# Kernel optimization log

Measured on AMD Instinct MI355X. Metric: run time of the kernel, lower is better.

## Reference

```python
import jax, jax.numpy as jnp
import numpy as np

H = 512          # hidden_size
E = 2 * H        # bidirectional embed dim
NH = 8           # attention heads
HD = E // NH     # head dim = 128
SEQ = 10         # hard-coded seq_len in forward
IN = 512         # input_size
OUT = 256        # output_size


def _gru_dir(gi, Whh, bhh, reverse):
    # gi: [B,S,3H] precomputed input-side gate pre-activations
    if reverse:
        gi = gi[:, ::-1]
    B = gi.shape[0]
    h0 = jnp.zeros((B, H), gi.dtype)

    def step(h, gi_t):
        gh = h @ Whh.T + bhh                      # [B,3H]
        ir, iz, inn = jnp.split(gi_t, 3, axis=-1)
        hr, hz, hn = jnp.split(gh, 3, axis=-1)
        r = jax.nn.sigmoid(ir + hr)
        z = jax.nn.sigmoid(iz + hz)
        n = jnp.tanh(inn + r * hn)
        h_new = (1.0 - z) * n + z * h
        return h_new, h_new

    _, hs = jax.lax.scan(step, h0, jnp.swapaxes(gi, 0, 1))
    hs = jnp.swapaxes(hs, 0, 1)                   # [B,S,H]
    if reverse:
        hs = hs[:, ::-1]
    return hs


def _bi_gru_layer(x_seq, Wih, Whh, bih, bhh):
    # Wih: [2, 3H, in]; dir 0 = forward, dir 1 = backward
    outs = []
    for d, rev in ((0, False), (1, True)):
        gi = jnp.einsum('bsi,gi->bsg', x_seq, Wih[d]) + bih[d]
        outs.append(_gru_dir(gi, Whh[d], bhh[d], rev))
    return jnp.concatenate(outs, axis=-1)         # [B,S,2H]


def _attention(x, in_proj_w, in_proj_b, out_proj_w, out_proj_b):
    B, S, _ = x.shape
    qkv = x @ in_proj_w.T + in_proj_b             # [B,S,3E]
    q, k, v = jnp.split(qkv, 3, axis=-1)
    q = q.reshape(B, S, NH, HD)
    k = k.reshape(B, S, NH, HD)
    v = v.reshape(B, S, NH, HD)
    scores = jnp.einsum('bqhd,bkhd->bhqk', q, k) / jnp.sqrt(jnp.asarray(HD, x.dtype))
    attn = jax.nn.softmax(scores, axis=-1)
    o = jnp.einsum('bhqk,bkhd->bqhd', attn, v).reshape(B, S, E)
    return o @ out_proj_w.T + out_proj_b


def _forward(x, Wp, bp, Wih0, Whh0, bih0, bhh0, Wih1, Whh1, bih1, bhh1,
             in_proj_w, in_proj_b, out_proj_w, out_proj_b, W1, b1, W2, b2):
    x_proj = x @ Wp.T + bp                        # [B,H]
    phases = 2.0 * np.pi * np.arange(SEQ) / SEQ
    cos = jnp.asarray(np.cos(phases), x.dtype)    # [S]
    sin = jnp.asarray(np.sin(phases), x.dtype)
    rolled = jnp.roll(x_proj, shift=1, axis=-1)
    x_seq = (x_proj[:, None, :] * (1.0 + 0.1 * cos[None, :, None])
             + 0.05 * sin[None, :, None] * rolled[:, None, :])  # [B,S,H]
    h1 = _bi_gru_layer(x_seq, Wih0, Whh0, bih0, bhh0)           # [B,S,2H]
    gru_out = _bi_gru_layer(h1, Wih1, Whh1, bih1, bhh1)         # [B,S,2H]
    attn_out = _attention(gru_out, in_proj_w, in_proj_b, out_proj_w, out_proj_b)
    aggregated = jnp.mean(gru_out + attn_out, axis=1)           # [B,2H]
    hid = jnp.tanh(aggregated @ W1.T + b1)                      # [B,128]
    return hid @ W2.T + b2                                      # [B,OUT]


def setup_inputs() -> dict:
    key = jax.random.key(0)
    ks = jax.random.split(key, 24)
    s = 1.0 / np.sqrt(H)
    u = lambda k, shape: jax.random.uniform(k, shape, jnp.float32, -s, s)
    return {
        'x': jax.random.normal(ks[0], (4096, IN), jnp.float32),
        'Wp': u(ks[1], (H, IN)), 'bp': u(ks[2], (H,)),
        'Wih0': u(ks[3], (2, 3 * H, H)), 'Whh0': u(ks[4], (2, 3 * H, H)),
        'bih0': u(ks[5], (2, 3 * H)), 'bhh0': u(ks[6], (2, 3 * H)),
        'Wih1': u(ks[7], (2, 3 * H, 2 * H)), 'Whh1': u(ks[8], (2, 3 * H, H)),
        'bih1': u(ks[9], (2, 3 * H)), 'bhh1': u(ks[10], (2, 3 * H)),
        'in_proj_w': u(ks[11], (3 * E, E)), 'in_proj_b': u(ks[12], (3 * E,)),
        'out_proj_w': u(ks[13], (E, E)), 'out_proj_b': u(ks[14], (E,)),
        'W1': u(ks[15], (128, E)), 'b1': u(ks[16], (128,)),
        'W2': u(ks[17], (OUT, 128)), 'b2': u(ks[18], (OUT,)),
    }


def reference(x, Wp, bp, Wih0, Whh0, bih0, bhh0, Wih1, Whh1, bih1, bhh1,
              in_proj_w, in_proj_b, out_proj_w, out_proj_b, W1, b1, W2, b2):
    return _forward(x, Wp, bp, Wih0, Whh0, bih0, bhh0, Wih1, Whh1, bih1, bhh1,
                    in_proj_w, in_proj_b, out_proj_w, out_proj_b, W1, b1, W2, b2)
```

## Files before the change

### kernel.cpp

```cpp
#include <hip/hip_runtime.h>
#include <math.h>


#define SEQ 10

typedef unsigned short bf16u;
typedef __attribute__((ext_vector_type(8))) short short8v;
typedef __attribute__((ext_vector_type(4))) float f32x4;

__device__ __forceinline__ float b2f(bf16u u) {
    union { unsigned int i; float f; } v; v.i = ((unsigned int)u) << 16; return v.f;
}
__device__ __forceinline__ bf16u f2b(float f) {
    union { float f; unsigned int i; } v; v.f = f;
    unsigned int r = (v.i + 0x7FFFu + ((v.i >> 16) & 1u)) >> 16;
    return (bf16u)r;
}
__device__ __forceinline__ float fast_sigm(float x) { return 1.0f / (1.0f + __expf(-x)); }
__device__ __forceinline__ float fast_tanh(float x) {
    float e = __expf(-2.0f * x);
    return 2.0f / (1.0f + e) - 1.0f;
}

__global__ void cvt_f2b(const float* __restrict__ src, bf16u* __restrict__ dst, int n4)
{
    int i = blockIdx.x * 256 + threadIdx.x;
    if (i < n4) {
        float4 v = ((const float4*)src)[i];
        ushort4 u; u.x = f2b(v.x); u.y = f2b(v.y); u.z = f2b(v.z); u.w = f2b(v.w);
        ((ushort4*)dst)[i] = u;
    }
}

template <typename TC>
__global__ __launch_bounds__(256) void gemm_mfma(
    const bf16u* __restrict__ A, long long sAz, int lda,
    const bf16u* __restrict__ W, long long sWz,
    const float* __restrict__ bias, long long sBz,
    TC* __restrict__ C, long long sCz, int ldc,
    int K, int act)
{
    __shared__ bf16u As[128 * 64];
    __shared__ bf16u Ws[128 * 64];

    const int z = blockIdx.z;
    A += (long long)z * sAz;
    W += (long long)z * sWz;
    C += (long long)z * sCz;
    const float* bz = bias ? (bias + (long long)z * sBz) : nullptr;

    const int gx = gridDim.x;
    const int nwg = gx * gridDim.y;
    const int orig = blockIdx.y * gx + blockIdx.x;
    const int q = nwg >> 3, rres = nwg & 7;
    const int xcd = orig & 7, loc = orig >> 3;
    const int wgid = (xcd < rres ? xcd * (q + 1) : rres * (q + 1) + (xcd - rres) * q) + loc;
    const int bm = (wgid / gx) * 128;
    const int bn = (wgid % gx) * 128;

    const int tid = threadIdx.x;
    const int lane = tid & 63;
    const int wave = tid >> 6;
    const int wr = (wave >> 1) * 64;
    const int wc = (wave & 1) * 64;
    const int l15 = lane & 15;
    const int lk8 = (lane >> 4) * 8;

    f32x4 acc[4][4];
#pragma unroll
    for (int i = 0; i < 4; ++i)
#pragma unroll
        for (int j = 0; j < 4; ++j)
#pragma unroll
            for (int r = 0; r < 4; ++r) acc[i][j][r] = 0.0f;

    const int sr = wave * 32 + (lane >> 3);
    const int sc = (lane & 7) * 8;
    const bf16u* Ag = A + (long long)(bm + sr) * lda + sc;
    const bf16u* Wg = W + (long long)(bn + sr) * K + sc;
    bf16u* Al = As + wave * 32 * 64;
    bf16u* Wl = Ws + wave * 32 * 64;

    for (int k0 = 0; k0 < K; k0 += 64) {
#pragma unroll
        for (int p = 0; p < 4; ++p) {
            __builtin_amdgcn_global_load_lds(
                (const __attribute__((address_space(1))) void*)(Ag + k0 + (long long)(8 * p) * lda),
                (__attribute__((address_space(3))) void*)(Al + 8 * p * 64), 16, 0, 0);
            __builtin_amdgcn_global_load_lds(
                (const __attribute__((address_space(1))) void*)(Wg + k0 + (long long)(8 * p) * K),
                (__attribute__((address_space(3))) void*)(Wl + 8 * p * 64), 16, 0, 0);
        }
        __syncthreads();
#pragma unroll
        for (int ks = 0; ks < 2; ++ks) {
            short8v af[4], bfr[4];
#pragma unroll
            for (int i = 0; i < 4; ++i)
                af[i] = *(const short8v*)(As + (wr + i * 16 + l15) * 64 + ks * 32 + lk8);
#pragma unroll
            for (int i = 0; i < 4; ++i)
                bfr[i] = *(const short8v*)(Ws + (wc + i * 16 + l15) * 64 + ks * 32 + lk8);
#pragma unroll
            for (int mi = 0; mi < 4; ++mi)
#pragma unroll
                for (int ni = 0; ni < 4; ++ni)
                    acc[mi][ni] = __builtin_amdgcn_mfma_f32_16x16x32_bf16(
                        af[mi], bfr[ni], acc[mi][ni], 0, 0, 0);
        }
        __syncthreads();
    }

    const int r0 = (lane >> 4) * 4;
#pragma unroll
    for (int mi = 0; mi < 4; ++mi) {
#pragma unroll
        for (int ni = 0; ni < 4; ++ni) {
            const int col = bn + wc + ni * 16 + l15;
            float badd = bz ? bz[col] : 0.0f;
#pragma unroll
            for (int r = 0; r < 4; ++r) {
                const long long row = bm + wr + mi * 16 + r0 + r;
                float v = acc[mi][ni][r] + badd;
                if (act) v = tanhf(v);
                if constexpr (sizeof(TC) == 4) ((float*)C)[row * ldc + col] = v;
                else                           ((bf16u*)C)[row * ldc + col] = f2b(v);
            }
        }
    }
}

template <int LAYER, bool FIRST>
__global__ __launch_bounds__(256) void gru_step(
    const bf16u* __restrict__ Hb,
    const bf16u* __restrict__ Whh,
    const float* __restrict__ bhh,
    const bf16u* __restrict__ P0,
    const bf16u* __restrict__ P1,
    const float* __restrict__ bih,
    const bf16u* __restrict__ GIT,
    const float* __restrict__ hprev,
    float* __restrict__ hnext,
    bf16u* __restrict__ hnextb,
    bf16u* __restrict__ hout,
    int t, int CB)
{
    __shared__ bf16u As[64 * 64];
    __shared__ bf16u Ws[96 * 64];

    const int z = blockIdx.z;
    const int bn = blockIdx.x * 32;
    const int bm = blockIdx.y * 64;
    const int tid = threadIdx.x;
    const int lane = tid & 63;
    const int wave = tid >> 6;
    const int wm = wave >> 1;
    const int wn = wave & 1;
    const int l15 = lane & 15;
    const int lk8 = (lane >> 4) * 8;

    f32x4 acc[3][2];
#pragma unroll
    for (int g = 0; g < 3; ++g)
#pragma unroll
        for (int i = 0; i < 2; ++i)
#pragma unroll
            for (int r = 0; r < 4; ++r) acc[g][i][r] = 0.0f;

    if constexpr (!FIRST) {
        const bf16u* hsrc = Hb + (long long)z * CB * 512;
        const bf16u* wsrc = Whh + (long long)z * 1536 * 512;

        const int sc = (lane & 7) * 8;
        const bf16u* Ag = hsrc + (long long)(bm + 16 * wave + (lane >> 3)) * 512 + sc;
        bf16u* Al = As + 16 * wave * 64;

        const bf16u* Wg[3];
#pragma unroll
        for (int p = 0; p < 3; ++p) {
            const int lr = 24 * wave + 8 * p + (lane >> 3);
            const int g = lr >> 5, c = lr & 31;
            Wg[p] = wsrc + (long long)(g * 512 + bn + c) * 512 + sc;
        }
        bf16u* Wl = Ws + 24 * wave * 64;

        for (int k0 = 0; k0 < 512; k0 += 64) {
#pragma unroll
            for (int p = 0; p < 2; ++p)
                __builtin_amdgcn_global_load_lds(
                    (const __attribute__((address_space(1))) void*)(Ag + k0 + (long long)(8 * p) * 512),
                    (__attribute__((address_space(3))) void*)(Al + 8 * p * 64), 16, 0, 0);
#pragma unroll
            for (int p = 0; p < 3; ++p)
                __builtin_amdgcn_global_load_lds(
                    (const __attribute__((address_space(1))) void*)(Wg[p] + k0),
                    (__attribute__((address_space(3))) void*)(Wl + 8 * p * 64), 16, 0, 0);
            __syncthreads();
#pragma unroll
            for (int ks = 0; ks < 2; ++ks) {
                short8v af[2], bf[3];
#pragma unroll
                for (int mi = 0; mi < 2; ++mi)
                    af[mi] = *(const short8v*)(As + (wm * 32 + mi * 16 + l15) * 64 + ks * 32 + lk8);
#pragma unroll
                for (int g = 0; g < 3; ++g)
                    bf[g] = *(const short8v*)(Ws + (g * 32 + wn * 16 + l15) * 64 + ks * 32 + lk8);
#pragma unroll
                for (int g = 0; g < 3; ++g)
#pragma unroll
                    for (int mi = 0; mi < 2; ++mi)
                        acc[g][mi] = __builtin_amdgcn_mfma_f32_16x16x32_bf16(
                            af[mi], bf[g], acc[g][mi], 0, 0, 0);
            }
            __syncthreads();
        }
    }

    const int r0 = (lane >> 4) * 4;
    const int s = z ? (SEQ - 1 - t) : t;
    float c0 = 0.0f, c1 = 0.0f;
    if (LAYER == 0) {
        float ph = 0.6283185307179586f * (float)s;
        c0 = 1.0f + 0.1f * cosf(ph);
        c1 = 0.05f * sinf(ph);
    }

    const int j = bn + wn * 16 + l15;
    const float bh0 = bhh[z * 1536 + j];
    const float bh1 = bhh[z * 1536 + 512 + j];
    const float bh2 = bhh[z * 1536 + 1024 + j];
    float bi0 = 0, bi1 = 0, bi2 = 0;
    if (LAYER == 0) {
        bi0 = bih[z * 1536 + j];
        bi1 = bih[z * 1536 + 512 + j];
        bi2 = bih[z * 1536 + 1024 + j];
    }

#pragma unroll
    for (int mi = 0; mi < 2; ++mi) {
#pragma unroll
        for (int rr = 0; rr < 4; ++rr) {
            const int m = bm + wm * 32 + mi * 16 + r0 + rr;
            float gr = acc[0][mi][rr] + bh0;
            float gz = acc[1][mi][rr] + bh1;
            float gn = acc[2][mi][rr] + bh2;
            float ir, iz, inn;
            if (LAYER == 0) {
                const bf16u* p0 = P0 + (long long)m * 3072 + z * 1536 + j;
                const bf16u* p1 = P1 + (long long)m * 3072 + z * 1536 + j;
                ir  = c0 * b2f(p0[0])    + c1 * b2f(p1[0])    + bi0;
                iz  = c0 * b2f(p0[512])  + c1 * b2f(p1[512])  + bi1;
                inn = c0 * b2f(p0[1024]) + c1 * b2f(p1[1024]) + bi2;
            } else {
                const bf16u* gi = GIT + (((long long)z * CB + m) * SEQ + s) * 1536 + j;
                ir = b2f(gi[0]); iz = b2f(gi[512]); inn = b2f(gi[1024]);
            }
            const long long ho = ((long long)z * CB + m) * 512 + j;
            float r  = fast_sigm(ir + gr);
            float zz = fast_sigm(iz + gz);
            float n  = fast_tanh(inn + r * gn);
            float hnew;
            if constexpr (FIRST) hnew = (1.0f - zz) * n;
            else                 hnew = (1.0f - zz) * n + zz * hprev[ho];
            hnext[ho]  = hnew;
            hnextb[ho] = f2b(hnew);
            hout[((long long)m * SEQ + s) * 1024 + z * 512 + j] = f2b(hnew);
        }
    }
}

__global__ void roll_b(const bf16u* __restrict__ xp, bf16u* __restrict__ rl)
{
    int idx = blockIdx.x * 256 + threadIdx.x;
    int i = idx & 511;
    int b = idx >> 9;
    rl[(size_t)b * 512 + i] = xp[(size_t)b * 512 + ((i + 511) & 511)];
}

__global__ __launch_bounds__(128) void attn_kernel(const bf16u* __restrict__ qkv,
                                                   bf16u* __restrict__ o)
{
    const int bh = blockIdx.x;
    const int h = bh & 7;
    const int bl = bh >> 3;
    const int tid = threadIdx.x;

    __shared__ float Q[SEQ][128], Kx[SEQ][128], V[SEQ][128], Amat[SEQ][SEQ];

    const bf16u* base = qkv + (size_t)bl * SEQ * 3072 + h * 128;
#pragma unroll
    for (int s = 0; s < SEQ; ++s) {
        Q[s][tid]  = b2f(base[s * 3072 + tid]);
        Kx[s][tid] = b2f(base[s * 3072 + 1024 + tid]);
        V[s][tid]  = b2f(base[s * 3072 + 2048 + tid]);
    }
    __syncthreads();

    if (tid < SEQ * SEQ) {
        int q = tid / SEQ, k = tid % SEQ;
        float acc = 0.0f;
#pragma unroll 8
        for (int d0 = 0; d0 < 128; ++d0) acc += Q[q][d0] * Kx[k][d0];
        Amat[q][k] = acc * 0.08838834764831845f;
    }
    __syncthreads();

    if (tid < SEQ) {
        float m = -1e30f;
#pragma unroll
        for (int k = 0; k < SEQ; ++k) m = fmaxf(m, Amat[tid][k]);
        float e[SEQ], ssum = 0.0f;
#pragma unroll
        for (int k = 0; k < SEQ; ++k) { e[k] = expf(Amat[tid][k] - m); ssum += e[k]; }
        float inv = 1.0f / ssum;
#pragma unroll
        for (int k = 0; k < SEQ; ++k) Amat[tid][k] = e[k] * inv;
    }
    __syncthreads();

    bf16u* ob = o + (size_t)bl * SEQ * 1024 + h * 128;
#pragma unroll
    for (int q = 0; q < SEQ; ++q) {
        float acc = 0.0f;
#pragma unroll
        for (int k = 0; k < SEQ; ++k) acc += Amat[q][k] * V[k][tid];
        ob[q * 1024 + tid] = f2b(acc);
    }
}

__global__ void mean_kernel(const bf16u* __restrict__ go, const bf16u* __restrict__ ao,
                            bf16u* __restrict__ agg)
{
    int idx = blockIdx.x * 256 + threadIdx.x;
    int j4 = (idx & 255) * 4;
    int bl = idx >> 8;
    const bf16u* g = go + (size_t)bl * (SEQ * 1024) + j4;
    const bf16u* a = ao + (size_t)bl * (SEQ * 1024) + j4;
    float s0 = 0, s1 = 0, s2 = 0, s3 = 0;
#pragma unroll
    for (int t = 0; t < SEQ; ++t) {
        ushort4 gv = *(const ushort4*)(g + t * 1024);
        ushort4 av = *(const ushort4*)(a + t * 1024);
        s0 += b2f(gv.x) + b2f(av.x);
        s1 += b2f(gv.y) + b2f(av.y);
        s2 += b2f(gv.z) + b2f(av.z);
        s3 += b2f(gv.w) + b2f(av.w);
    }
    ushort4 u; u.x = f2b(0.1f * s0); u.y = f2b(0.1f * s1); u.z = f2b(0.1f * s2); u.w = f2b(0.1f * s3);
    *(ushort4*)(agg + (size_t)bl * 1024 + j4) = u;
}

extern "C" void kernel_launch(void* const* d_in, const int* in_sizes, int n_in,
                              void* d_out, int out_size, void* d_ws, size_t ws_size,
                              hipStream_t stream)
{
    const float* x    = (const float*)d_in[0];
    const float* Wp   = (const float*)d_in[1];
    const float* bp   = (const float*)d_in[2];
    const float* Wih0 = (const float*)d_in[3];
    const float* Whh0 = (const float*)d_in[4];
    const float* bih0 = (const float*)d_in[5];
    const float* bhh0 = (const float*)d_in[6];
    const float* Wih1 = (const float*)d_in[7];
    const float* Whh1 = (const float*)d_in[8];
    const float* bih1 = (const float*)d_in[9];
    const float* bhh1 = (const float*)d_in[10];
    const float* ipw  = (const float*)d_in[11];
    const float* ipb  = (const float*)d_in[12];
    const float* opw  = (const float*)d_in[13];
    const float* opb  = (const float*)d_in[14];
    const float* W1   = (const float*)d_in[15];
    const float* b1   = (const float*)d_in[16];
    const float* W2   = (const float*)d_in[17];
    const float* b2   = (const float*)d_in[18];
    float* out = (float*)d_out;

    const long long WOVER = 9437184LL;
    const long long WALL  = 24969216LL;
    int CB = 0;
    for (int c = 4096; c >= 128; c >>= 1)
        if (WOVER + (long long)c * 114688 <= (long long)ws_size) { CB = c; break; }
    if (CB == 0) return;
    const bool resident = (WALL + (long long)CB * 114688 <= (long long)ws_size);
    const long long WB = resident ? WALL : WOVER;
    const int CBA = CB / 2;

    bf16u* wreg = (bf16u*)d_ws;
    bf16u *Wpb, *Wih0b, *Whh0b, *Wih1b, *Whh1b, *ipwb, *opwb, *W1b, *W2b;
    if (resident) {
        Wpb   = wreg;
        Wih0b = wreg + 262144;
        Whh0b = wreg + 1835008;
        Wih1b = wreg + 3407872;
        Whh1b = wreg + 6553600;
        ipwb  = wreg + 8126464;
        opwb  = wreg + 11272192;
        W1b   = wreg + 12320768;
        W2b   = wreg + 12451840;
    } else {
        Wpb   = wreg;
        Wih0b = wreg + 262144;
        Whh0b = wreg + 1835008;
        Wih1b = wreg;
        Whh1b = wreg + 3145728;
        ipwb  = wreg;
        opwb  = wreg + 3145728;
        W1b   = wreg + 4194304;
        W2b   = wreg + 4325376;
    }

    char* A0 = (char*)d_ws + WB;
    bf16u* H1c = (bf16u*)A0;
    bf16u* GOc = (bf16u*)(A0 + 20480LL * CB);
    char*  U   = A0 + 40960LL * CB;
    bf16u* P0    = (bf16u*)U;
    bf16u* P1    = (bf16u*)(U + 6144LL * CB);
    bf16u* XB    = (bf16u*)(U + 12288LL * CB);
    bf16u* XPb   = (bf16u*)(U + 13312LL * CB);
    bf16u* RLb   = (bf16u*)(U + 14336LL * CB);
    bf16u* GIT   = (bf16u*)U;
    char*  HC    = U + 61440LL * CB;
    bf16u* QKV   = (bf16u*)U;
    bf16u* OC    = (bf16u*)(U + 61440LL * CB);
    bf16u* AOC   = (bf16u*)A0;
    bf16u* AGGb  = (bf16u*)(A0 + 10240LL * CB);
    bf16u* HIDb  = (bf16u*)(A0 + 12288LL * CB);

    const dim3 blk(256);
    const int MB = CB / 128;

    auto cvt = [&](const float* s, bf16u* d, long long nfloats) {
        int n4 = (int)(nfloats / 4);
        cvt_f2b<<<(n4 + 255) / 256, blk, 0, stream>>>(s, d, n4);
    };

    if (resident) {
        cvt(Wp,   Wpb,   512LL * 512);
        cvt(Wih0, Wih0b, 2LL * 1536 * 512);
        cvt(Whh0, Whh0b, 2LL * 1536 * 512);
        cvt(Wih1, Wih1b, 2LL * 1536 * 1024);
        cvt(Whh1, Whh1b, 2LL * 1536 * 512);
        cvt(ipw,  ipwb,  3072LL * 1024);
        cvt(opw,  opwb,  1024LL * 1024);
        cvt(W1,   W1b,   128LL * 1024);
        cvt(W2,   W2b,   256LL * 128);
    }

    for (int c0 = 0; c0 < 4096; c0 += CB) {
        cvt(x + (long long)c0 * 512, XB, (long long)CB * 512);
        if (!resident) {
            cvt(Wp,   Wpb,   512LL * 512);
            cvt(Wih0, Wih0b, 2LL * 1536 * 512);
            cvt(Whh0, Whh0b, 2LL * 1536 * 512);
        }

        gemm_mfma<bf16u><<<dim3(4, MB, 1), blk, 0, stream>>>(
            XB, 0, 512, Wpb, 0, bp, 0, XPb, 0, 512, 512, 0);
        roll_b<<<CB * 2, blk, 0, stream>>>(XPb, RLb);
        gemm_mfma<bf16u><<<dim3(24, MB, 2), blk, 0, stream>>>(
            XPb, (long long)CB * 512, 512, Wih0b, 0, nullptr, 0,
            P0, (long long)CB * 3072, 3072, 512, 0);

        for (int t = 0; t < SEQ; ++t) {
            const int rb = t & 1;
            float* hprev  = (float*)(HC + (long long)rb * 6144 * CB);
            bf16u* Hbr    = (bf16u*)(HC + (long long)rb * 6144 * CB + 4096LL * CB);
            float* hnext  = (float*)(HC + (long long)(1 - rb) * 6144 * CB);
            bf16u* hnextb = (bf16u*)(HC + (long long)(1 - rb) * 6144 * CB + 4096LL * CB);
            if (t == 0)
                gru_step<0, true><<<dim3(16, CB / 64, 2), blk, 0, stream>>>(
                    Hbr, Whh0b, bhh0, P0, P1, bih0, nullptr,
                    hprev, hnext, hnextb, H1c, t, CB);
            else
                gru_step<0, false><<<dim3(16, CB / 64, 2), blk, 0, stream>>>(
                    Hbr, Whh0b, bhh0, P0, P1, bih0, nullptr,
                    hprev, hnext, hnextb, H1c, t, CB);
        }

        if (!resident) {
            cvt(Wih1, Wih1b, 2LL * 1536 * 1024);
            cvt(Whh1, Whh1b, 2LL * 1536 * 512);
        }
        gemm_mfma<bf16u><<<dim3(12, MB * 10, 2), blk, 0, stream>>>(
            H1c, 0, 1024, Wih1b, 1536LL * 1024, bih1, 1536,
            GIT, (long long)CB * SEQ * 1536, 1536, 1024, 0);

        for (int t = 0; t < SEQ; ++t) {
            const int rb = t & 1;
            float* hprev  = (float*)(HC + (long long)rb * 6144 * CB);
            bf16u* Hbr    = (bf16u*)(HC + (long long)rb * 6144 * CB + 4096LL * CB);
            float* hnext  = (float*)(HC + (long long)(1 - rb) * 6144 * CB);
            bf16u* hnextb = (bf16u*)(HC + (long long)(1 - rb) * 6144 * CB + 4096LL * CB);
            if (t == 0)
                gru_step<1, true><<<dim3(16, CB / 64, 2), blk, 0, stream>>>(
                    Hbr, Whh1b, bhh1, nullptr, nullptr, nullptr, GIT,
                    hprev, hnext, hnextb, GOc, t, CB);
            else
                gru_step<1, false><<<dim3(16, CB / 64, 2), blk, 0, stream>>>(
                    Hbr, Whh1b, bhh1, nullptr, nullptr, nullptr, GIT,
                    hprev, hnext, hnextb, GOc, t, CB);
        }

        if (!resident) {
            cvt(ipw, ipwb, 3072LL * 1024);
            cvt(opw, opwb, 1024LL * 1024);
            cvt(W1,  W1b,  128LL * 1024);
            cvt(W2,  W2b,  256LL * 128);
        }
        gemm_mfma<bf16u><<<dim3(24, MB * 10, 1), blk, 0, stream>>>(
            GOc, 0, 1024, ipwb, 0, ipb, 0, QKV, 0, 3072, 1024, 0);
        for (int a0 = 0; a0 < CB; a0 += CBA) {
            attn_kernel<<<CBA * 8, dim3(128), 0, stream>>>(
                QKV + (long long)a0 * 30720, OC);
            gemm_mfma<bf16u><<<dim3(8, CBA * 10 / 128, 1), blk, 0, stream>>>(
                OC, 0, 1024, opwb, 0, opb, 0, AOC, 0, 1024, 1024, 0);
            mean_kernel<<<CBA, blk, 0, stream>>>(
                GOc + (long long)a0 * 10240, AOC, AGGb + (long long)a0 * 1024);
        }
        gemm_mfma<bf16u><<<dim3(1, MB, 1), blk, 0, stream>>>(
            AGGb, 0, 1024, W1b, 0, b1, 0, HIDb, 0, 128, 1024, 1);
        gemm_mfma<float><<<dim3(2, MB, 1), blk, 0, stream>>>(
            HIDb, 0, 128, W2b, 0, b2, 0, out + (long long)c0 * 256, 0, 256, 128, 0);
    }
}
```

Measured before the change: 2.379 ms.

## Add 256x256 double-buffered MFMA GEMM with XCD remap for large projections

Introduces a 512-thread GEMM kernel with 256x256 output tiles, double-buffered LDS staging that prefetches the next K tile while computing the current one, and a workgroup-id remap that groups neighbouring tiles on the same XCD. It replaces the 128x128 GEMM for the layer-1 input projection and the attention QKV projection. The aim is more operand reuse per loaded byte, overlap of global loads with MFMA work, and better L2 locality. The cost is 128KB of LDS and many accumulators per block, so occupancy drops, and M must be a multiple of 256 (CB*10/256).

```diff
diff --git a/kernel.cpp b/kernel.cpp
--- a/kernel.cpp
+++ b/kernel.cpp
@@ -7,6 +7,9 @@
 typedef unsigned short bf16u;
 typedef __attribute__((ext_vector_type(8))) short short8v;
 typedef __attribute__((ext_vector_type(4))) float f32x4;
+
+#define AS1 __attribute__((address_space(1)))
+#define AS3 __attribute__((address_space(3)))
 
 __device__ __forceinline__ float b2f(bf16u u) {
     union { unsigned int i; float f; } v; v.i = ((unsigned int)u) << 16; return v.f;
@@ -29,6 +32,122 @@
         float4 v = ((const float4*)src)[i];
         ushort4 u; u.x = f2b(v.x); u.y = f2b(v.y); u.z = f2b(v.z); u.w = f2b(v.w);
         ((ushort4*)dst)[i] = u;
+    }
+}
+
+template <typename TC>
+__global__ __launch_bounds__(512) void gemm_mfma256(
+    const bf16u* __restrict__ A, long long sAz, int lda,
+    const bf16u* __restrict__ W, long long sWz,
+    const float* __restrict__ bias, long long sBz,
+    TC* __restrict__ C, long long sCz, int ldc,
+    int K, int act)
+{
+    __shared__ bf16u As[2][256 * 64];
+    __shared__ bf16u Ws[2][256 * 64];
+
+    const int z = blockIdx.z;
+    A += (long long)z * sAz;
+    W += (long long)z * sWz;
+    C += (long long)z * sCz;
+    const float* bz = bias ? (bias + (long long)z * sBz) : nullptr;
+
+    const int gx = gridDim.x;
+    const int nwg = gx * gridDim.y;
+    const int orig = blockIdx.y * gx + blockIdx.x;
+    const int q = nwg >> 3, rres = nwg & 7;
+    const int xcd = orig & 7, loc = orig >> 3;
+    const int wgid = (xcd < rres ? xcd * (q + 1) : rres * (q + 1) + (xcd - rres) * q) + loc;
+    const int bm = (wgid / gx) * 256;
+    const int bn = (wgid % gx) * 256;
+
+    const int tid = threadIdx.x;
+    const int lane = tid & 63;
+    const int w = tid >> 6;
+    const int wm = w >> 2;
+    const int wn = w & 3;
+    const int l15 = lane & 15;
+    const int lk8 = (lane >> 4) * 8;
+
+    f32x4 acc[8][4];
+#pragma unroll
+    for (int i = 0; i < 8; ++i)
+#pragma unroll
+        for (int j = 0; j < 4; ++j)
+#pragma unroll
+            for (int r = 0; r < 4; ++r) acc[i][j][r] = 0.0f;
+
+    const int srow = lane >> 3;
+    const int scol = (lane & 7) * 8;
+    const bf16u* Ag[4];
+    const bf16u* Wg[4];
+    int loff[4];
+#pragma unroll
+    for (int p = 0; p < 4; ++p) {
+        const int r = p * 64 + w * 8 + srow;
+        Ag[p] = A + (long long)(bm + r) * lda + scol;
+        Wg[p] = W + (long long)(bn + r) * K + scol;
+        loff[p] = (p * 8 + w) * 512;
+    }
+
+    const int nt = K >> 6;
+
+#pragma unroll
+    for (int p = 0; p < 4; ++p) {
+        __builtin_amdgcn_global_load_lds((const AS1 void*)(Ag[p]),
+            (AS3 void*)(&As[0][loff[p]]), 16, 0, 0);
+        __builtin_amdgcn_global_load_lds((const AS1 void*)(Wg[p]),
+            (AS3 void*)(&Ws[0][loff[p]]), 16, 0, 0);
+    }
+    __syncthreads();
+
+    for (int t = 0; t < nt; ++t) {
+        const int pb = t & 1;
+        if (t + 1 < nt) {
+            const int k1 = (t + 1) << 6;
+#pragma unroll
+            for (int p = 0; p < 4; ++p) {
+                __builtin_amdgcn_global_load_lds((const AS1 void*)(Ag[p] + k1),
+                    (AS3 void*)(&As[1 - pb][loff[p]]), 16, 0, 0);
+                __builtin_amdgcn_global_load_lds((const AS1 void*)(Wg[p] + k1),
+                    (AS3 void*)(&Ws[1 - pb][loff[p]]), 16, 0, 0);
+            }
+        }
+#pragma unroll
+        for (int ks = 0; ks < 2; ++ks) {
+            short8v af[8], bfr[4];
+#pragma unroll
+            for (int i = 0; i < 8; ++i)
+                af[i] = *(const short8v*)(&As[pb][(wm * 128 + i * 16 + l15) * 64 + ks * 32 + lk8]);
+#pragma unroll
+            for (int i = 0; i < 4; ++i)
+                bfr[i] = *(const short8v*)(&Ws[pb][(wn * 64 + i * 16 + l15) * 64 + ks * 32 + lk8]);
+#pragma unroll
+            for (int mi = 0; mi < 8; ++mi)
+#pragma unroll
+                for (int ni = 0; ni < 4; ++ni)
+                    acc[mi][ni] = __builtin_amdgcn_mfma_f32_16x16x32_bf16(
+                        af[mi], bfr[ni], acc[mi][ni], 0, 0, 0);
+        }
+        __syncthreads();
+    }
+
+    const int r0 = (lane >> 4) * 4;
+#pragma unroll
+    for (int mi = 0; mi < 8; ++mi) {
+#pragma unroll
+        for (int ni = 0; ni < 4; ++ni) {
+            const int col = bn + wn * 64 + ni * 16 + l15;
+            float badd = bz ? bz[col] : 0.0f;
+#pragma unroll
+            for (int r = 0; r < 4; ++r) {
+                const long long row = bm + wm * 128 + mi * 16 + r0 + r;
+                float v = acc[mi][ni][r] + badd;
+                if (act) v = tanhf(v);
+                if constexpr (sizeof(TC) == 4) ((float*)C)[row * ldc + col] = v;
+                else                           ((bf16u*)C)[row * ldc + col] = f2b(v);
+            }
+        }
     }
 }
 
@@ -85,11 +204,11 @@
 #pragma unroll
         for (int p = 0; p < 4; ++p) {
             __builtin_amdgcn_global_load_lds(
-                (const __attribute__((address_space(1))) void*)(Ag + k0 + (long long)(8 * p) * lda),
-                (__attribute__((address_space(3))) void*)(Al + 8 * p * 64), 16, 0, 0);
+                (const AS1 void*)(Ag + k0 + (long long)(8 * p) * lda),
+                (AS3 void*)(Al + 8 * p * 64), 16, 0, 0);
             __builtin_amdgcn_global_load_lds(
-                (const __attribute__((address_space(1))) void*)(Wg + k0 + (long long)(8 * p) * K),
-                (__attribute__((address_space(3))) void*)(Wl + 8 * p * 64), 16, 0, 0);
+                (const AS1 void*)(Wg + k0 + (long long)(8 * p) * K),
+                (AS3 void*)(Wl + 8 * p * 64), 16, 0, 0);
         }
         __syncthreads();
 #pragma unroll
@@ -188,13 +307,13 @@
 #pragma unroll
             for (int p = 0; p < 2; ++p)
                 __builtin_amdgcn_global_load_lds(
-                    (const __attribute__((address_space(1))) void*)(Ag + k0 + (long long)(8 * p) * 512),
-                    (__attribute__((address_space(3))) void*)(Al + 8 * p * 64), 16, 0, 0);
+                    (const AS1 void*)(Ag + k0 + (long long)(8 * p) * 512),
+                    (AS3 void*)(Al + 8 * p * 64), 16, 0, 0);
 #pragma unroll
             for (int p = 0; p < 3; ++p)
                 __builtin_amdgcn_global_load_lds(
-                    (const __attribute__((address_space(1))) void*)(Wg[p] + k0),
-                    (__attribute__((address_space(3))) void*)(Wl + 8 * p * 64), 16, 0, 0);
+                    (const AS1 void*)(Wg[p] + k0),
+                    (AS3 void*)(Wl + 8 * p * 64), 16, 0, 0);
             __syncthreads();
 #pragma unroll
             for (int ks = 0; ks < 2; ++ks) {
@@ -481,7 +600,7 @@
             cvt(Wih1, Wih1b, 2LL * 1536 * 1024);
             cvt(Whh1, Whh1b, 2LL * 1536 * 512);
         }
-        gemm_mfma<bf16u><<<dim3(12, MB * 10, 2), blk, 0, stream>>>(
+        gemm_mfma256<bf16u><<<dim3(6, CB * 10 / 256, 2), dim3(512), 0, stream>>>(
             H1c, 0, 1024, Wih1b, 1536LL * 1024, bih1, 1536,
             GIT, (long long)CB * SEQ * 1536, 1536, 1024, 0);
 
@@ -507,7 +626,7 @@
             cvt(W1,  W1b,  128LL * 1024);
             cvt(W2,  W2b,  256LL * 128);
         }
-        gemm_mfma<bf16u><<<dim3(24, MB * 10, 1), blk, 0, stream>>>(
+        gemm_mfma256<bf16u><<<dim3(12, CB * 10 / 256, 1), dim3(512), 0, stream>>>(
             GOc, 0, 1024, ipwb, 0, ipb, 0, QKV, 0, 3072, 1024, 0);
         for (int a0 = 0; a0 < CB; a0 += CBA) {
             attn_kernel<<<CBA * 8, dim3(128), 0, stream>>>(
```

New measurement: 2.302 ms. -3.2%, faster.
